# Kernel optimization log

Measured on AMD Instinct MI355X. Metric: run time of the kernel, lower is better.

Reference implementation:

```python
import jax, jax.numpy as jnp
import numpy as np

A, N, D, H, ADIM = 8, 32768, 128, 4, 32  # agents, batch, hidden, heads, attend_dim


def setup_inputs() -> dict:
    key = jax.random.key(0)
    ks = jax.random.split(key, 7)
    querys = jax.random.normal(ks[0], (A, N, D), jnp.float32)
    keys = jax.random.normal(ks[1], (A, N, D), jnp.float32)
    values = jax.random.normal(ks[2], (A, N, D), jnp.float32)
    s = 1.0 / np.sqrt(D)
    Wk = jax.random.normal(ks[3], (H, ADIM, D), jnp.float32) * s   # key_extractors (no bias)
    Wsel = jax.random.normal(ks[4], (H, ADIM, D), jnp.float32) * s  # selector_extractors (no bias)
    Wv = jax.random.normal(ks[5], (H, ADIM, D), jnp.float32) * s   # value_extractors Linear
    bv = jax.random.normal(ks[6], (H, ADIM), jnp.float32) * s      # value_extractors bias
    return {"querys": querys, "keys": keys, "values": values,
            "Wk": Wk, "Wsel": Wsel, "Wv": Wv, "bv": bv}


def _offdiag_idx(a):
    # idx[i, j] enumerates the a-1 agents != i, in order (matches torch list comp j != a_i)
    j = jnp.arange(a - 1)[None, :]
    i = jnp.arange(a)[:, None]
    return jnp.where(j < i, j, j + 1)  # [A, A-1]


def reference(querys, keys, values, Wk, Wsel, Wv, bv):
    # per-head projections: [H, A, N, K]
    hk = jnp.einsum('and,hkd->hank', keys, Wk)
    hs = jnp.einsum('and,hkd->hank', querys, Wsel)
    hv = jax.nn.leaky_relu(jnp.einsum('and,hkd->hank', values, Wv) + bv[:, None, None, :],
                           negative_slope=0.01)
    # full logits over all key-agents j for each query-agent i: [H, A, N, A]
    logits_full = jnp.einsum('hink,hjnk->hinj', hs, hk)
    scale = 1.0 / jnp.sqrt(jnp.asarray(hk.shape[-1], hk.dtype))
    # self-exclusion: mask j == i so softmax over j equals softmax over the other agents
    self_mask = jnp.eye(A, dtype=bool)[None, :, None, :]
    probs_full = jax.nn.softmax(jnp.where(self_mask, -1e9, logits_full * scale), axis=-1)
    # attended values: [H, A, N, K] (diagonal prob is exactly 0 after masking? it is ~e^{-1e9} ~ 0)
    other = jnp.einsum('hinj,hjnk->hink', probs_full, hv)
    # gather the self-excluded logits/probs in the original (A-1)-length layout
    idx = _offdiag_idx(A)
    idx4 = jnp.broadcast_to(idx[None, :, None, :], logits_full.shape[:-1] + (A - 1,))
    logits_ex = jnp.take_along_axis(logits_full, idx4, axis=-1)  # [H, A, N, A-1]
    probs_ex = jnp.take_along_axis(probs_full, idx4, axis=-1)    # [H, A, N, A-1]
    # reorder to agent-major like the torch nested lists: [A, H, ...]
    return (jnp.swapaxes(other, 0, 1),
            jnp.swapaxes(logits_ex, 0, 1),
            jnp.swapaxes(probs_ex, 0, 1))
```

## Files before the change

kernel.cpp:

```cpp
#include <hip/hip_runtime.h>
#include <hip/hip_bf16.h>

typedef unsigned short u16;
typedef unsigned int u32;

#define AGT 8
#define NBATCH 32768
#define DDIM 128
#define HEADS 4
#define KDIM 32

typedef float f32x4 __attribute__((ext_vector_type(4)));
typedef __bf16 bf16x8 __attribute__((ext_vector_type(8)));
typedef short s16x8 __attribute__((ext_vector_type(8)));
typedef u32 u32x4 __attribute__((ext_vector_type(4)));

union FragU { s16x8 s; bf16x8 b; u32x4 u; };

__device__ __forceinline__ u16 f2bf(float f) {
  u32 u = __float_as_uint(f);
  u = (u + 0x7FFFu + ((u >> 16) & 1u)) >> 16;
  return (u16)u;
}

__device__ __forceinline__ u32 packbf(float lo, float hi) {
  return (u32)f2bf(lo) | ((u32)f2bf(hi) << 16);
}

__global__ void prep_weights(const float* __restrict__ Wk,
                             const float* __restrict__ Ws,
                             const float* __restrict__ Wv,
                             u16* __restrict__ Wb) {
  int idx = blockIdx.x * 256 + threadIdx.x;
  if (idx >= 3 * 8 * 4 * 64 * 8) return;
  int b  = idx & 7;
  int l  = (idx >> 3) & 63;
  int kc = (idx >> 9) & 3;
  int t  = (idx >> 11) & 7;
  int pj = idx >> 14;
  int c = t * 16 + (l & 15);
  int h = c >> 5, kk = c & 31;
  int d = kc * 32 + ((b >> 2) << 4) + ((l >> 4) << 2) + (b & 3);
  const float* W = (pj == 0) ? Wk : ((pj == 1) ? Ws : Wv);
  Wb[idx] = f2bf(W[(h * KDIM + kk) * DDIM + d]);
}

__device__ __forceinline__ void load_pack_row(const float* __restrict__ rowp,
                                              int lg, FragU f[4]) {
#pragma unroll
  for (int kc = 0; kc < 4; ++kc) {
    const float4 x0 = *(const float4*)(rowp + kc * 32 + lg * 4);
    const float4 x1 = *(const float4*)(rowp + kc * 32 + lg * 4 + 16);
    u32x4 t;
    t[0] = packbf(x0.x, x0.y);
    t[1] = packbf(x0.z, x0.w);
    t[2] = packbf(x1.x, x1.y);
    t[3] = packbf(x1.z, x1.w);
    f[kc].u = t;
  }
}

__global__ __launch_bounds__(256, 2) void fused_attn(
    const float* __restrict__ qin, const float* __restrict__ kin,
    const float* __restrict__ vin, const u16* __restrict__ Wb,
    const float* __restrict__ bv,
    float* __restrict__ out0, float* __restrict__ out1,
    float* __restrict__ out2) {
  const int tid = threadIdx.x;
  const int l = tid & 63;
  const int w = tid >> 6;
  const int lr = l & 15;
  const int lg = l >> 4;
  const int n_base = blockIdx.x * 8 + w * 2;
  const int my_agent = lr >> 1;
  const int my_n = n_base + (lr & 1);
  const size_t xoff = ((size_t)my_agent * NBATCH + (size_t)my_n) * DDIM;

  const f32x4 zero4 = (f32x4)(0.0f);

  FragU hk4[HEADS];
  {
    FragU fx[4];
    load_pack_row(kin + xoff, lg, fx);
    f32x4 a[8];
#pragma unroll
    for (int mt = 0; mt < 8; ++mt) {
      a[mt] = zero4;
#pragma unroll
      for (int kc = 0; kc < 4; ++kc) {
        FragU fb;
        fb.s = *(const s16x8*)(Wb + ((((0 * 8 + mt) * 4 + kc) * 64 + l) << 3));
        a[mt] = __builtin_amdgcn_mfma_f32_16x16x32_bf16(fb.b, fx[kc].b, a[mt],
                                                        0, 0, 0);
      }
    }
#pragma unroll
    for (int h = 0; h < HEADS; ++h) {
      u32x4 t;
      t[0] = packbf(a[2 * h][0], a[2 * h][1]);
      t[1] = packbf(a[2 * h][2], a[2 * h][3]);
      t[2] = packbf(a[2 * h + 1][0], a[2 * h + 1][1]);
      t[3] = packbf(a[2 * h + 1][2], a[2 * h + 1][3]);
      hk4[h].u = t;
    }
  }

  FragU hs4[HEADS];
  {
    FragU fx[4];
    load_pack_row(qin + xoff, lg, fx);
    f32x4 a[8];
#pragma unroll
    for (int mt = 0; mt < 8; ++mt) {
      a[mt] = zero4;
#pragma unroll
      for (int kc = 0; kc < 4; ++kc) {
        FragU fb;
        fb.s = *(const s16x8*)(Wb + ((((1 * 8 + mt) * 4 + kc) * 64 + l) << 3));
        a[mt] = __builtin_amdgcn_mfma_f32_16x16x32_bf16(fb.b, fx[kc].b, a[mt],
                                                        0, 0, 0);
      }
    }
#pragma unroll
    for (int h = 0; h < HEADS; ++h) {
      u32x4 t;
      t[0] = packbf(a[2 * h][0], a[2 * h][1]);
      t[1] = packbf(a[2 * h][2], a[2 * h][3]);
      t[2] = packbf(a[2 * h + 1][0], a[2 * h + 1][1]);
      t[3] = packbf(a[2 * h + 1][2], a[2 * h + 1][3]);
      hs4[h].u = t;
    }
  }

  FragU hv4[8];
  {
    FragU fx[4];
    load_pack_row(vin + xoff, lg, fx);
#pragma unroll
    for (int ct = 0; ct < 8; ++ct) {
      f32x4 a = zero4;
#pragma unroll
      for (int kc = 0; kc < 4; ++kc) {
        FragU fb;
        fb.s = *(const s16x8*)(Wb + ((((2 * 8 + ct) * 4 + kc) * 64 + l) << 3));
        a = __builtin_amdgcn_mfma_f32_16x16x32_bf16(fx[kc].b, fb.b, a, 0, 0, 0);
      }
      const float bias = bv[ct * 16 + lr];
      float x[4];
#pragma unroll
      for (int rg = 0; rg < 4; ++rg) {
        float v = a[rg] + bias;
        x[rg] = (v > 0.0f) ? v : 0.01f * v;
      }
      u32x4 t;
      t[0] = packbf(x[0], x[1]);
      t[1] = packbf(x[2], x[3]);
      t[2] = 0;
      t[3] = 0;
      hv4[ct].u = t;
    }
  }

  const float scale = 0.17677669529663687f;
  const int ipar = lr & 1;

#pragma unroll
  for (int h = 0; h < HEADS; ++h) {
    f32x4 S = __builtin_amdgcn_mfma_f32_16x16x32_bf16(hk4[h].b, hs4[h].b,
                                                      zero4, 0, 0, 0);
    float sl[4];
#pragma unroll
    for (int rg = 0; rg < 4; ++rg) {
      const int jrow = 4 * lg + rg;
      const bool valid = ((rg & 1) == ipar) && (jrow != lr);
      sl[rg] = valid ? S[rg] * scale : -1e30f;
    }
    float mp = fmaxf(fmaxf(sl[0], sl[1]), fmaxf(sl[2], sl[3]));
    mp = fmaxf(mp, __shfl_xor(mp, 16));
    mp = fmaxf(mp, __shfl_xor(mp, 32));
    float e[4];
    float sp = 0.0f;
#pragma unroll
    for (int rg = 0; rg < 4; ++rg) {
      e[rg] = __expf(sl[rg] - mp);
      sp += e[rg];
    }
    sp += __shfl_xor(sp, 16);
    sp += __shfl_xor(sp, 32);
    const float inv = 1.0f / sp;
    float p[4];
#pragma unroll
    for (int rg = 0; rg < 4; ++rg) p[rg] = e[rg] * inv;

    const int a_i = lr >> 1;
    const int n = n_base + ipar;
    const size_t ob7 = ((size_t)(a_i * HEADS + h) * NBATCH + (size_t)n) * 7;
#pragma unroll
    for (int rg = 0; rg < 4; ++rg) {
      const int jrow = 4 * lg + rg;
      if (((rg & 1) == ipar) && (jrow != lr)) {
        const int a_j = jrow >> 1;
        const int jj = a_j - ((a_j > a_i) ? 1 : 0);
        out1[ob7 + jj] = S[rg];
        out2[ob7 + jj] = p[rg];
      }
    }

    FragU P;
    {
      u32x4 t;
      t[0] = packbf(p[0], p[1]);
      t[1] = packbf(p[2], p[3]);
      t[2] = 0;
      t[3] = 0;
      P.u = t;
    }
    f32x4 O0 = __builtin_amdgcn_mfma_f32_16x16x32_bf16(P.b, hv4[2 * h].b,
                                                       zero4, 0, 0, 0);
    f32x4 O1 = __builtin_amdgcn_mfma_f32_16x16x32_bf16(P.b, hv4[2 * h + 1].b,
                                                       zero4, 0, 0, 0);
#pragma unroll
    for (int rg = 0; rg < 4; ++rg) {
      const int irow = 4 * lg + rg;
      const int a_o = irow >> 1;
      const int n_o = n_base + (irow & 1);
      const size_t o0 =
          ((size_t)(a_o * HEADS + h) * NBATCH + (size_t)n_o) * KDIM;
      out0[o0 + lr] = O0[rg];
      out0[o0 + 16 + lr] = O1[rg];
    }
  }
}

extern "C" void kernel_launch(void* const* d_in, const int* in_sizes, int n_in,
                              void* d_out, int out_size, void* d_ws,
                              size_t ws_size, hipStream_t stream) {
  const float* qin = (const float*)d_in[0];
  const float* kin = (const float*)d_in[1];
  const float* vin = (const float*)d_in[2];
  const float* Wk  = (const float*)d_in[3];
  const float* Ws  = (const float*)d_in[4];
  const float* Wv  = (const float*)d_in[5];
  const float* bvp = (const float*)d_in[6];

  float* out0 = (float*)d_out;
  float* out1 = out0 + (size_t)AGT * HEADS * NBATCH * KDIM;
  float* out2 = out1 + (size_t)AGT * HEADS * NBATCH * 7;

  u16* Wb = (u16*)d_ws;

  prep_weights<<<dim3(192), dim3(256), 0, stream>>>(Wk, Ws, Wv, Wb);
  fused_attn<<<dim3(NBATCH / 8), dim3(256), 0, stream>>>(
      qin, kin, vin, Wb, bvp, out0, out1, out2);
}
```

Before: 272.0 us.

## Loop each wave over four batch pairs with register-prefetched inputs

Each wave now handles four iterations of two batch rows instead of one, with the next iteration's K/Q/V rows loaded into registers while the current iteration's projections and softmax run. The grid shrinks from 4096 to 1024 blocks, bias values are hoisted into registers, and manual bf16 rounding is replaced by native __bf16 conversions. This is meant to hide global load latency behind MFMA work. In exchange it raises register pressure under the 2-blocks-per-CU launch bound and reduces the number of blocks available for occupancy.

Result: slower. 631.1 us (+132.0%).

```diff
diff --git a/kernel.cpp b/kernel.cpp
--- a/kernel.cpp
+++ b/kernel.cpp
@@ -21,10 +21,6 @@
   u32 u = __float_as_uint(f);
   u = (u + 0x7FFFu + ((u >> 16) & 1u)) >> 16;
   return (u16)u;
-}
-
-__device__ __forceinline__ u32 packbf(float lo, float hi) {
-  return (u32)f2bf(lo) | ((u32)f2bf(hi) << 16);
 }
 
 __global__ void prep_weights(const float* __restrict__ Wk,
@@ -45,18 +41,84 @@
   Wb[idx] = f2bf(W[(h * KDIM + kk) * DDIM + d]);
 }
 
-__device__ __forceinline__ void load_pack_row(const float* __restrict__ rowp,
-                                              int lg, FragU f[4]) {
+__device__ __forceinline__ void issue8(const float* __restrict__ rowp, int lg,
+                                       float4 r[8]) {
 #pragma unroll
   for (int kc = 0; kc < 4; ++kc) {
-    const float4 x0 = *(const float4*)(rowp + kc * 32 + lg * 4);
-    const float4 x1 = *(const float4*)(rowp + kc * 32 + lg * 4 + 16);
-    u32x4 t;
-    t[0] = packbf(x0.x, x0.y);
-    t[1] = packbf(x0.z, x0.w);
-    t[2] = packbf(x1.x, x1.y);
-    t[3] = packbf(x1.z, x1.w);
-    f[kc].u = t;
+    r[kc * 2]     = *(const float4*)(rowp + kc * 32 + lg * 4);
+    r[kc * 2 + 1] = *(const float4*)(rowp + kc * 32 + lg * 4 + 16);
+  }
+}
+
+__device__ __forceinline__ void cvt8(const float4 r[8], FragU f[4]) {
+#pragma unroll
+  for (int kc = 0; kc < 4; ++kc) {
+    const float4 x0 = r[kc * 2];
+    const float4 x1 = r[kc * 2 + 1];
+    FragU t;
+    t.b[0] = (__bf16)x0.x; t.b[1] = (__bf16)x0.y;
+    t.b[2] = (__bf16)x0.z; t.b[3] = (__bf16)x0.w;
+    t.b[4] = (__bf16)x1.x; t.b[5] = (__bf16)x1.y;
+    t.b[6] = (__bf16)x1.z; t.b[7] = (__bf16)x1.w;
+    f[kc] = t;
+  }
+}
+
+template <int PJ>
+__device__ __forceinline__ void projT(const FragU fx[4],
+                                      const u16* __restrict__ Wb, int l,
+                                      FragU out4[HEADS]) {
+  const f32x4 zero4 = (f32x4)(0.0f);
+#pragma unroll
+  for (int g = 0; g < 2; ++g) {
+    f32x4 a[4];
+#pragma unroll
+    for (int m4 = 0; m4 < 4; ++m4) {
+      a[m4] = zero4;
+      const int mt = g * 4 + m4;
+#pragma unroll
+      for (int kc = 0; kc < 4; ++kc) {
+        FragU fb;
+        fb.s = *(const s16x8*)(Wb + ((((PJ * 8 + mt) * 4 + kc) * 64 + l) << 3));
+        a[m4] = __builtin_amdgcn_mfma_f32_16x16x32_bf16(fb.b, fx[kc].b, a[m4],
+                                                        0, 0, 0);
+      }
+    }
+#pragma unroll
+    for (int hh = 0; hh < 2; ++hh) {
+      FragU t;
+      t.b[0] = (__bf16)a[2 * hh][0];     t.b[1] = (__bf16)a[2 * hh][1];
+      t.b[2] = (__bf16)a[2 * hh][2];     t.b[3] = (__bf16)a[2 * hh][3];
+      t.b[4] = (__bf16)a[2 * hh + 1][0]; t.b[5] = (__bf16)a[2 * hh + 1][1];
+      t.b[6] = (__bf16)a[2 * hh + 1][2]; t.b[7] = (__bf16)a[2 * hh + 1][3];
+      out4[g * 2 + hh] = t;
+    }
+  }
+}
+
+__device__ __forceinline__ void projV(const FragU fx[4],
+                                      const u16* __restrict__ Wb, int l,
+                                      const float biasr[8], FragU hv4[8]) {
+  const f32x4 zero4 = (f32x4)(0.0f);
+#pragma unroll
+  for (int ct = 0; ct < 8; ++ct) {
+    f32x4 a = zero4;
+#pragma unroll
+    for (int kc = 0; kc < 4; ++kc) {
+      FragU fb;
+      fb.s = *(const s16x8*)(Wb + ((((2 * 8 + ct) * 4 + kc) * 64 + l) << 3));
+      a = __builtin_amdgcn_mfma_f32_16x16x32_bf16(fx[kc].b, fb.b, a, 0, 0, 0);
+    }
+    FragU t;
+#pragma unroll
+    for (int rg = 0; rg < 4; ++rg) {
+      float v = a[rg] + biasr[ct];
+      v = (v > 0.0f) ? v : 0.01f * v;
+      t.b[rg] = (__bf16)v;
+    }
+    t.u[2] = 0;
+    t.u[3] = 0;
+    hv4[ct] = t;
   }
 }
 
@@ -71,163 +133,115 @@
   const int w = tid >> 6;
   const int lr = l & 15;
   const int lg = l >> 4;
-  const int n_base = blockIdx.x * 8 + w * 2;
+  const int gw = blockIdx.x * 4 + w;
+  const int nw = gw * 8;
   const int my_agent = lr >> 1;
-  const int my_n = n_base + (lr & 1);
-  const size_t xoff = ((size_t)my_agent * NBATCH + (size_t)my_n) * DDIM;
+  const int ipar = lr & 1;
+  const size_t xoff =
+      ((size_t)my_agent * NBATCH + (size_t)(nw + ipar)) * DDIM;
+  const float* pk = kin + xoff;
+  const float* pq = qin + xoff;
+  const float* pv = vin + xoff;
+
+  float biasr[8];
+#pragma unroll
+  for (int ct = 0; ct < 8; ++ct) biasr[ct] = bv[ct * 16 + lr];
+
+  float4 rK[8], rQ[8], rV[8];
+  issue8(pk, lg, rK);
+  issue8(pq, lg, rQ);
+  issue8(pv, lg, rV);
 
   const f32x4 zero4 = (f32x4)(0.0f);
-
-  FragU hk4[HEADS];
-  {
-    FragU fx[4];
-    load_pack_row(kin + xoff, lg, fx);
-    f32x4 a[8];
-#pragma unroll
-    for (int mt = 0; mt < 8; ++mt) {
-      a[mt] = zero4;
-#pragma unroll
-      for (int kc = 0; kc < 4; ++kc) {
-        FragU fb;
-        fb.s = *(const s16x8*)(Wb + ((((0 * 8 + mt) * 4 + kc) * 64 + l) << 3));
-        a[mt] = __builtin_amdgcn_mfma_f32_16x16x32_bf16(fb.b, fx[kc].b, a[mt],
-                                                        0, 0, 0);
-      }
-    }
+  const float scale = 0.17677669529663687f;
+
+  for (int it = 0; it < 4; ++it) {
+    FragU fxK[4], fxQ[4], fxV[4];
+    cvt8(rK, fxK);
+    cvt8(rQ, fxQ);
+    cvt8(rV, fxV);
+
+    FragU hk4[HEADS], hs4[HEADS], hv4[8];
+    projT<0>(fxK, Wb, l, hk4);
+    projT<1>(fxQ, Wb, l, hs4);
+    projV(fxV, Wb, l, biasr, hv4);
+
+    if (it < 3) {
+      pk += 2 * DDIM;
+      pq += 2 * DDIM;
+      pv += 2 * DDIM;
+      issue8(pk, lg, rK);
+      issue8(pq, lg, rQ);
+      issue8(pv, lg, rV);
+    }
+
+    f32x4 S[HEADS];
+#pragma unroll
+    for (int h = 0; h < HEADS; ++h)
+      S[h] = __builtin_amdgcn_mfma_f32_16x16x32_bf16(hk4[h].b, hs4[h].b,
+                                                     zero4, 0, 0, 0);
+
+    const int n_i = nw + it * 2 + ipar;
+    const int a_i = my_agent;
+
 #pragma unroll
     for (int h = 0; h < HEADS; ++h) {
-      u32x4 t;
-      t[0] = packbf(a[2 * h][0], a[2 * h][1]);
-      t[1] = packbf(a[2 * h][2], a[2 * h][3]);
-      t[2] = packbf(a[2 * h + 1][0], a[2 * h + 1][1]);
-      t[3] = packbf(a[2 * h + 1][2], a[2 * h + 1][3]);
-      hk4[h].u = t;
-    }
-  }
-
-  FragU hs4[HEADS];
-  {
-    FragU fx[4];
-    load_pack_row(qin + xoff, lg, fx);
-    f32x4 a[8];
-#pragma unroll
-    for (int mt = 0; mt < 8; ++mt) {
-      a[mt] = zero4;
-#pragma unroll
-      for (int kc = 0; kc < 4; ++kc) {
-        FragU fb;
-        fb.s = *(const s16x8*)(Wb + ((((1 * 8 + mt) * 4 + kc) * 64 + l) << 3));
-        a[mt] = __builtin_amdgcn_mfma_f32_16x16x32_bf16(fb.b, fx[kc].b, a[mt],
-                                                        0, 0, 0);
-      }
-    }
-#pragma unroll
-    for (int h = 0; h < HEADS; ++h) {
-      u32x4 t;
-      t[0] = packbf(a[2 * h][0], a[2 * h][1]);
-      t[1] = packbf(a[2 * h][2], a[2 * h][3]);
-      t[2] = packbf(a[2 * h + 1][0], a[2 * h + 1][1]);
-      t[3] = packbf(a[2 * h + 1][2], a[2 * h + 1][3]);
-      hs4[h].u = t;
-    }
-  }
-
-  FragU hv4[8];
-  {
-    FragU fx[4];
-    load_pack_row(vin + xoff, lg, fx);
-#pragma unroll
-    for (int ct = 0; ct < 8; ++ct) {
-      f32x4 a = zero4;
-#pragma unroll
-      for (int kc = 0; kc < 4; ++kc) {
-        FragU fb;
-        fb.s = *(const s16x8*)(Wb + ((((2 * 8 + ct) * 4 + kc) * 64 + l) << 3));
-        a = __builtin_amdgcn_mfma_f32_16x16x32_bf16(fx[kc].b, fb.b, a, 0, 0, 0);
-      }
-      const float bias = bv[ct * 16 + lr];
-      float x[4];
-#pragma unroll
-      for (int rg = 0; rg < 4; ++rg) {
-        float v = a[rg] + bias;
-        x[rg] = (v > 0.0f) ? v : 0.01f * v;
-      }
-      u32x4 t;
-      t[0] = packbf(x[0], x[1]);
-      t[1] = packbf(x[2], x[3]);
-      t[2] = 0;
-      t[3] = 0;
-      hv4[ct].u = t;
-    }
-  }
-
-  const float scale = 0.17677669529663687f;
-  const int ipar = lr & 1;
-
-#pragma unroll
-  for (int h = 0; h < HEADS; ++h) {
-    f32x4 S = __builtin_amdgcn_mfma_f32_16x16x32_bf16(hk4[h].b, hs4[h].b,
-                                                      zero4, 0, 0, 0);
-    float sl[4];
-#pragma unroll
-    for (int rg = 0; rg < 4; ++rg) {
-      const int jrow = 4 * lg + rg;
-      const bool valid = ((rg & 1) == ipar) && (jrow != lr);
-      sl[rg] = valid ? S[rg] * scale : -1e30f;
-    }
-    float mp = fmaxf(fmaxf(sl[0], sl[1]), fmaxf(sl[2], sl[3]));
-    mp = fmaxf(mp, __shfl_xor(mp, 16));
-    mp = fmaxf(mp, __shfl_xor(mp, 32));
-    float e[4];
-    float sp = 0.0f;
-#pragma unroll
-    for (int rg = 0; rg < 4; ++rg) {
-      e[rg] = __expf(sl[rg] - mp);
-      sp += e[rg];
-    }
-    sp += __shfl_xor(sp, 16);
-    sp += __shfl_xor(sp, 32);
-    const float inv = 1.0f / sp;
-    float p[4];
-#pragma unroll
-    for (int rg = 0; rg < 4; ++rg) p[rg] = e[rg] * inv;
-
-    const int a_i = lr >> 1;
-    const int n = n_base + ipar;
-    const size_t ob7 = ((size_t)(a_i * HEADS + h) * NBATCH + (size_t)n) * 7;
-#pragma unroll
-    for (int rg = 0; rg < 4; ++rg) {
-      const int jrow = 4 * lg + rg;
-      if (((rg & 1) == ipar) && (jrow != lr)) {
-        const int a_j = jrow >> 1;
-        const int jj = a_j - ((a_j > a_i) ? 1 : 0);
-        out1[ob7 + jj] = S[rg];
-        out2[ob7 + jj] = p[rg];
-      }
-    }
-
-    FragU P;
-    {
-      u32x4 t;
-      t[0] = packbf(p[0], p[1]);
-      t[1] = packbf(p[2], p[3]);
-      t[2] = 0;
-      t[3] = 0;
-      P.u = t;
-    }
-    f32x4 O0 = __builtin_amdgcn_mfma_f32_16x16x32_bf16(P.b, hv4[2 * h].b,
-                                                       zero4, 0, 0, 0);
-    f32x4 O1 = __builtin_amdgcn_mfma_f32_16x16x32_bf16(P.b, hv4[2 * h + 1].b,
-                                                       zero4, 0, 0, 0);
-#pragma unroll
-    for (int rg = 0; rg < 4; ++rg) {
-      const int irow = 4 * lg + rg;
-      const int a_o = irow >> 1;
-      const int n_o = n_base + (irow & 1);
-      const size_t o0 =
-          ((size_t)(a_o * HEADS + h) * NBATCH + (size_t)n_o) * KDIM;
-      out0[o0 + lr] = O0[rg];
-      out0[o0 + 16 + lr] = O1[rg];
+      float sl[4];
+#pragma unroll
+      for (int rg = 0; rg < 4; ++rg) {
+        const int jrow = 4 * lg + rg;
+        const bool valid = ((rg & 1) == ipar) && (jrow != lr);
+        sl[rg] = valid ? S[h][rg] * scale : -1e30f;
+      }
+      float mp = fmaxf(fmaxf(sl[0], sl[1]), fmaxf(sl[2], sl[3]));
+      mp = fmaxf(mp, __shfl_xor(mp, 16));
+      mp = fmaxf(mp, __shfl_xor(mp, 32));
+      float e[4];
+      float sp = 0.0f;
+#pragma unroll
+      for (int rg = 0; rg < 4; ++rg) {
+        e[rg] = __expf(sl[rg] - mp);
+        sp += e[rg];
+      }
+      sp += __shfl_xor(sp, 16);
+      sp += __shfl_xor(sp, 32);
+      const float inv = 1.0f / sp;
+      float p[4];
+#pragma unroll
+      for (int rg = 0; rg < 4; ++rg) p[rg] = e[rg] * inv;
+
+      const size_t ob7 =
+          ((size_t)(a_i * HEADS + h) * NBATCH + (size_t)n_i) * 7;
+#pragma unroll
+      for (int rg = 0; rg < 4; ++rg) {
+        const int jrow = 4 * lg + rg;
+        if (((rg & 1) == ipar) && (jrow != lr)) {
+          const int a_j = jrow >> 1;
+          const int jj = a_j - ((a_j > a_i) ? 1 : 0);
+          out1[ob7 + jj] = S[h][rg];
+          out2[ob7 + jj] = p[rg];
+        }
+      }
+
+      FragU P;
+      P.b[0] = (__bf16)p[0]; P.b[1] = (__bf16)p[1];
+      P.b[2] = (__bf16)p[2]; P.b[3] = (__bf16)p[3];
+      P.u[2] = 0;
+      P.u[3] = 0;
+      f32x4 O0 = __builtin_amdgcn_mfma_f32_16x16x32_bf16(P.b, hv4[2 * h].b,
+                                                         zero4, 0, 0, 0);
+      f32x4 O1 = __builtin_amdgcn_mfma_f32_16x16x32_bf16(P.b, hv4[2 * h + 1].b,
+                                                         zero4, 0, 0, 0);
+#pragma unroll
+      for (int rg = 0; rg < 4; ++rg) {
+        const int irow = 4 * lg + rg;
+        const int a_o = irow >> 1;
+        const int n_o = nw + it * 2 + (irow & 1);
+        const size_t o0 =
+            ((size_t)(a_o * HEADS + h) * NBATCH + (size_t)n_o) * KDIM;
+        out0[o0 + lr] = O0[rg];
+        out0[o0 + 16 + lr] = O1[rg];
+      }
     }
   }
 }
@@ -250,6 +264,6 @@
   u16* Wb = (u16*)d_ws;
 
   prep_weights<<<dim3(192), dim3(256), 0, stream>>>(Wk, Ws, Wv, Wb);
-  fused_attn<<<dim3(NBATCH / 8), dim3(256), 0, stream>>>(
+  fused_attn<<<dim3(1024), dim3(256), 0, stream>>>(
       qin, kin, vin, Wb, bvp, out0, out1, out2);
 }
```
